# Kernel tuning notes

Hardware: AMD Instinct MI355X
Metric: run time of the kernel (lower is better)

## Reference

```python
import jax, jax.numpy as jnp
import numpy as np

C = 512
GROUPS = 8
EPS = 1e-5


def setup_inputs() -> dict:
    key = jax.random.key(0)
    ks = jax.random.split(key, 7)
    B, H, W = 16, 32, 32
    x = jax.random.normal(ks[0], (B, C, H, W), dtype=jnp.float32)
    gamma = jnp.ones((C,), jnp.float32)
    beta = jnp.zeros((C,), jnp.float32)
    # 1x1 convs stored as [out, in] matrices
    w_qkv = jax.random.normal(ks[1], (3 * C, C), dtype=jnp.float32) * (1.0 / np.sqrt(C))
    b_qkv = jax.random.normal(ks[2], (3 * C,), dtype=jnp.float32) * 0.02
    w_proj = jax.random.normal(ks[3], (C, C), dtype=jnp.float32) * (1.0 / np.sqrt(C))
    b_proj = jax.random.normal(ks[4], (C,), dtype=jnp.float32) * 0.02
    return {"x": x, "gamma": gamma, "beta": beta, "w_qkv": w_qkv,
            "b_qkv": b_qkv, "w_proj": w_proj, "b_proj": b_proj}


def _group_norm(x, gamma, beta):
    B, Cc, H, W = x.shape
    xg = x.reshape(B, GROUPS, Cc // GROUPS, H, W)
    mean = xg.mean(axis=(2, 3, 4), keepdims=True)
    var = xg.var(axis=(2, 3, 4), keepdims=True)
    xg = (xg - mean) * jax.lax.rsqrt(var + EPS)
    x = xg.reshape(B, Cc, H, W)
    return x * gamma[None, :, None, None] + beta[None, :, None, None]


def reference(x, gamma, beta, w_qkv, b_qkv, w_proj, b_proj):
    B, Cc, H, W = x.shape
    N = H * W
    h = _group_norm(x, gamma, beta)  # [B,C,H,W]
    hf = h.reshape(B, Cc, N)  # [B,C,N]
    # 1x1 conv == matmul over channel dim
    qkv = jnp.einsum('oc,bcn->bon', w_qkv, hf) + b_qkv[None, :, None]  # [B,3C,N]
    q, k, v = jnp.split(qkv, 3, axis=1)  # each [B,C,N]
    scale = 1.0 / jnp.sqrt(jnp.float32(Cc))
    # attn[b,i,j] = sum_c q[b,c,i] * k[b,c,j]
    attn = jnp.einsum('bci,bcj->bij', q, k) * scale  # [B,N,N]
    attn = jax.nn.softmax(attn, axis=-1)
    out = jnp.einsum('bij,bcj->bci', attn, v)  # [B,C,N]
    out = jnp.einsum('oc,bcn->bon', w_proj, out) + b_proj[None, :, None]
    return x + out.reshape(B, Cc, H, W)
```

## Files before the change

kernel.cpp:

```cpp
#include <hip/hip_runtime.h>
#include <hip/hip_bf16.h>

typedef unsigned short u16;
typedef unsigned int u32;
typedef __attribute__((ext_vector_type(8))) short short8;
typedef __attribute__((ext_vector_type(4))) float floatx4;

#define BATCH 16
#define CDIM 512
#define NSPAT 1024
#define NGROUP 8

__device__ __forceinline__ u16 f2bf(float f) {
    unsigned u = __float_as_uint(f);
    u += 0x7FFFu + ((u >> 16) & 1u);
    return (u16)(u >> 16);
}
__device__ __forceinline__ u32 f2bf2(float lo, float hi) {
    __hip_bfloat162 h = __float22bfloat162_rn(make_float2(lo, hi));
    return *(u32*)&h;
}

__device__ __forceinline__ void load_lds16(const void* g, void* l) {
    __builtin_amdgcn_global_load_lds(
        (const __attribute__((address_space(1))) unsigned int*)g,
        (__attribute__((address_space(3))) unsigned int*)l, 16, 0, 0);
}

__global__ __launch_bounds__(256) void prep_kernel(
    const float* __restrict__ w_qkv, const float* __restrict__ w_proj,
    const float* __restrict__ b_qkv, const float* __restrict__ x,
    u16* __restrict__ wmega, u16* __restrict__ wproj_bf, u16* __restrict__ wv_t,
    float* __restrict__ stats, float* __restrict__ lsums, float* __restrict__ bpv) {
    int b = blockIdx.x;
    int tid = threadIdx.x;
    if (b < 768) {
        const float* src = (b < 512) ? w_qkv : w_proj;
        u16* dst = (b < 512) ? wmega : wproj_bf;
        int i = (b < 512 ? b : b - 512) * 256 + tid;
        float4 v = ((const float4*)src)[i];
        u32* d = (u32*)dst;
        d[i * 2] = f2bf2(v.x, v.y);
        d[i * 2 + 1] = f2bf2(v.z, v.w);
        return;
    }
    if (b < 832) {
        __shared__ u16 t[64 * 66];
        int bt = b - 768;
        int tx = bt & 7, ty = bt >> 3;
        const float* src = w_qkv + (size_t)(1024 + ty * 64) * CDIM + tx * 64;
#pragma unroll
        for (int p = 0; p < 4; ++p) {
            int r = p * 16 + (tid >> 4);
            int c4 = (tid & 15) << 2;
            float4 v = *(const float4*)(src + (size_t)r * CDIM + c4);
            u16* d = &t[r * 66 + c4];
            d[0] = f2bf(v.x); d[1] = f2bf(v.y); d[2] = f2bf(v.z); d[3] = f2bf(v.w);
        }
        __syncthreads();
        u16* dst = wv_t + (size_t)(tx * 64) * CDIM + ty * 64;
#pragma unroll
        for (int p = 0; p < 4; ++p) {
            int c = p * 16 + (tid >> 4);
            int r4 = (tid & 15) << 2;
            ushort4 o;
            o.x = t[(r4 + 0) * 66 + c];
            o.y = t[(r4 + 1) * 66 + c];
            o.z = t[(r4 + 2) * 66 + c];
            o.w = t[(r4 + 3) * 66 + c];
            *(ushort4*)(dst + (size_t)c * CDIM + r4) = o;
        }
        return;
    }
    if (b < 960) {
        __shared__ float rs[4], rss[4];
        int bg = b - 832;
        const float4* xv = (const float4*)(x + (size_t)bg * 65536);
        float s = 0.f, ss = 0.f;
        for (int i = tid; i < 16384; i += 256) {
            float4 v = xv[i];
            s += v.x + v.y + v.z + v.w;
            ss += v.x * v.x + v.y * v.y + v.z * v.z + v.w * v.w;
        }
#pragma unroll
        for (int off = 32; off; off >>= 1) { s += __shfl_down(s, off); ss += __shfl_down(ss, off); }
        int wave = tid >> 6, lane = tid & 63;
        if (lane == 0) { rs[wave] = s; rss[wave] = ss; }
        __syncthreads();
        if (tid == 0) {
            float S1 = rs[0] + rs[1] + rs[2] + rs[3];
            float S2 = rss[0] + rss[1] + rss[2] + rss[3];
            float mean = S1 * (1.f / 65536.f);
            float var = S2 * (1.f / 65536.f) - mean * mean;
            stats[bg * 2] = mean;
            stats[bg * 2 + 1] = rsqrtf(var + 1e-5f);
        }
        return;
    }
    if (b < 976) {
        ((float4*)lsums)[(b - 960) * 256 + tid] = (float4){0.f, 0.f, 0.f, 0.f};
        return;
    }
    {
        int o0 = (b - 976) * 64;
        int wave = tid >> 6, lane = tid & 63;
        const float4* bvv = (const float4*)(b_qkv + 1024);
        float4 v0 = bvv[lane * 2], v1 = bvv[lane * 2 + 1];
        for (int it = 0; it < 16; ++it) {
            int o = o0 + wave * 16 + it;
            const float4* wr = (const float4*)(w_proj + (size_t)o * CDIM);
            float4 a0 = wr[lane * 2], a1 = wr[lane * 2 + 1];
            float s = a0.x * v0.x + a0.y * v0.y + a0.z * v0.z + a0.w * v0.w
                    + a1.x * v1.x + a1.y * v1.y + a1.z * v1.z + a1.w * v1.w;
#pragma unroll
            for (int off = 32; off; off >>= 1) s += __shfl_down(s, off);
            if (lane == 0) bpv[o] = s;
        }
    }
}

__device__ __forceinline__ void stage_tile(
    const u16* __restrict__ Ab, const u16* __restrict__ Bb, int lda, int ldb,
    int m0, int n0, int k0, u16* As, u16* Bs) {
    int tid = threadIdx.x;
#pragma unroll
    for (int it = 0; it < 4; ++it) {
        int c = it * 256 + tid;
        int r = c >> 3, p = c & 7;
        int kc = p ^ (r & 7);
        load_lds16(Ab + (size_t)(m0 + r) * lda + k0 + (kc << 3), &As[c << 3]);
        load_lds16(Bb + (size_t)(n0 + r) * ldb + k0 + (kc << 3), &Bs[c << 3]);
    }
}

__device__ __forceinline__ void compute_tile(
    const u16* As, const u16* Bs, int wm, int wn, int quad, int lrow,
    floatx4 (&acc)[4][4]) {
#pragma unroll
    for (int s = 0; s < 2; ++s) {
        short8 af[4], bf[4];
#pragma unroll
        for (int i = 0; i < 4; ++i) {
            int R = wm + i * 16 + lrow;
            int p = (s * 4 + quad) ^ (R & 7);
            af[i] = *(const short8*)&As[(R << 6) + (p << 3)];
        }
#pragma unroll
        for (int j = 0; j < 4; ++j) {
            int R = wn + j * 16 + lrow;
            int p = (s * 4 + quad) ^ (R & 7);
            bf[j] = *(const short8*)&Bs[(R << 6) + (p << 3)];
        }
#pragma unroll
        for (int i = 0; i < 4; ++i)
#pragma unroll
            for (int j = 0; j < 4; ++j)
                acc[i][j] = __builtin_amdgcn_mfma_f32_16x16x32_bf16(af[i], bf[j], acc[i][j], 0, 0, 0);
    }
}

__device__ __forceinline__ void gemm_core_sb(
    const u16* __restrict__ Ab, const u16* __restrict__ Bb, int K, int lda, int ldb,
    int m0, int n0, u16* As, u16* Bs, floatx4 (&acc)[4][4]) {
    int tid = threadIdx.x;
    int lane = tid & 63, wave = tid >> 6, quad = lane >> 4, lrow = lane & 15;
    int wm = (wave >> 1) << 6, wn = (wave & 1) << 6;
    for (int k0 = 0; k0 < K; k0 += 64) {
        stage_tile(Ab, Bb, lda, ldb, m0, n0, k0, As, Bs);
        __syncthreads();
        compute_tile(As, Bs, wm, wn, quad, lrow, acc);
        __syncthreads();
    }
}

#define ACC_INIT floatx4 acc[4][4]; \
    _Pragma("unroll") for (int i = 0; i < 4; ++i) \
    _Pragma("unroll") for (int j = 0; j < 4; ++j) acc[i][j] = (floatx4){0.f, 0.f, 0.f, 0.f};

#define EPILOG_IDX int lane = threadIdx.x & 63, wave = threadIdx.x >> 6; \
    int quad = lane >> 4, lrow = lane & 15; \
    int wm = (wave >> 1) << 6, wn = (wave & 1) << 6;

#define TSA 16384
#define TSB 8192

__device__ __forceinline__ void issueA(
    const u16* __restrict__ Ab, int lda, int m0, int t, int h, u16* smem) {
    int tid = threadIdx.x;
    u16* base = smem + (t & 1) * TSA + h * 8192;
#pragma unroll
    for (int l = 0; l < 2; ++l) {
        int c = l * 512 + tid;
        int ridx = c >> 3, p = c & 7;
        int kc = p ^ (ridx & 7);
        int r = ((ridx >> 6) << 7) + (h << 6) + (ridx & 63);
        load_lds16(Ab + (size_t)(m0 + r) * lda + (t << 6) + (kc << 3), base + (c << 3));
    }
}

__device__ __forceinline__ void issueB(
    const u16* __restrict__ Bb, int ldb, int n0, int t, int h, u16* smem) {
    int tid = threadIdx.x;
    u16* base = smem + 2 * TSA + (t & 1) * TSB + h * 4096;
    int ridx = tid >> 3, p = tid & 7;
    int kc = p ^ (ridx & 7);
    int r = ((ridx >> 4) << 5) + (h << 4) + (ridx & 15);
    load_lds16(Bb + (size_t)(n0 + r) * ldb + (t << 6) + (kc << 3), base + (tid << 3));
}

__device__ __forceinline__ void comp_phase(
    const u16* smem, int slot, int qm, int qn,
    int wrow, int wcol, int quad, int lrow, floatx4 (&acc)[8][2]) {
    const u16* Abase = smem + slot * TSA + qm * 8192;
    const u16* Bbase = smem + 2 * TSA + slot * TSB + qn * 4096;
    short8 af[8];
    short8 bf[2];
#pragma unroll
    for (int ks = 0; ks < 2; ++ks) {
#pragma unroll
        for (int i = 0; i < 4; ++i) {
            int ridx = wrow * 64 + i * 16 + lrow;
            int p = (ks * 4 + quad) ^ (ridx & 7);
            af[ks * 4 + i] = *(const short8*)&Abase[(ridx << 6) + (p << 3)];
        }
        int ridxb = wcol * 16 + lrow;
        int pb = (ks * 4 + quad) ^ (ridxb & 7);
        bf[ks] = *(const short8*)&Bbase[(ridxb << 6) + (pb << 3)];
    }
    asm volatile("s_waitcnt lgkmcnt(0)" ::: "memory");
    __builtin_amdgcn_sched_barrier(0);
    __builtin_amdgcn_s_setprio(1);
#pragma unroll
    for (int ks = 0; ks < 2; ++ks)
#pragma unroll
        for (int i = 0; i < 4; ++i)
            acc[qm * 4 + i][qn] = __builtin_amdgcn_mfma_f32_16x16x32_bf16(
                af[ks * 4 + i], bf[ks], acc[qm * 4 + i][qn], 0, 0, 0);
    __builtin_amdgcn_s_setprio(0);
}

#define PHASE_BAR  __builtin_amdgcn_s_barrier(); __builtin_amdgcn_sched_barrier(0);

__device__ __forceinline__ void gemm256(
    const u16* __restrict__ Ab, const u16* __restrict__ Bb, int K, int lda, int ldb,
    int m0, int n0, u16* smem, floatx4 (&acc)[8][2]) {
    int tid = threadIdx.x;
    int lane = tid & 63, wave = tid >> 6;
    int quad = lane >> 4, lrow = lane & 15;
    int wrow = wave >> 2, wcol = wave & 3;
    int nt = K >> 6;
    issueA(Ab, lda, m0, 0, 0, smem);
    issueA(Ab, lda, m0, 0, 1, smem);
    issueB(Bb, ldb, n0, 0, 0, smem);
    issueB(Bb, ldb, n0, 0, 1, smem);
    issueA(Ab, lda, m0, 1, 0, smem);
    issueB(Bb, ldb, n0, 1, 0, smem);
    for (int t = 0; t < nt; ++t) {
        int slot = t & 1;
        if (t + 1 < nt) { asm volatile("s_waitcnt vmcnt(3)" ::: "memory"); }
        else            { asm volatile("s_waitcnt vmcnt(0)" ::: "memory"); }
        PHASE_BAR;
        if (t + 1 < nt) issueA(Ab, lda, m0, t + 1, 1, smem);
        comp_phase(smem, slot, 0, 0, wrow, wcol, quad, lrow, acc);
        PHASE_BAR;
        if (t + 1 < nt) issueB(Bb, ldb, n0, t + 1, 1, smem);
        comp_phase(smem, slot, 0, 1, wrow, wcol, quad, lrow, acc);
        PHASE_BAR;
        if (t + 2 < nt) issueA(Ab, lda, m0, t + 2, 0, smem);
        comp_phase(smem, slot, 1, 0, wrow, wcol, quad, lrow, acc);
        PHASE_BAR;
        if (t + 2 < nt) issueB(Bb, ldb, n0, t + 2, 0, smem);
        comp_phase(smem, slot, 1, 1, wrow, wcol, quad, lrow, acc);
    }
    __builtin_amdgcn_sched_barrier(0);
}

#define ACC_INIT8 floatx4 acc[8][2]; \
    _Pragma("unroll") for (int i = 0; i < 8; ++i) \
    _Pragma("unroll") for (int j = 0; j < 2; ++j) acc[i][j] = (floatx4){0.f, 0.f, 0.f, 0.f};

#define EPILOG_IDX8 int lane = threadIdx.x & 63, wave = threadIdx.x >> 6; \
    int quad = lane >> 4, lrow = lane & 15; \
    int wrow = wave >> 2, wcol = wave & 3;

#define TSTR 66
__global__ __launch_bounds__(256) void gn_wpv_kernel(
    const float* __restrict__ x, const float* __restrict__ gamma, const float* __restrict__ beta,
    const float* __restrict__ stats, u16* __restrict__ hT,
    const u16* __restrict__ wproj_bf, const u16* __restrict__ wv_t, u16* __restrict__ wmega) {
    __shared__ u16 smem[2 * 128 * 64];
    int tid = threadIdx.x;
    if (blockIdx.z == 16) {
        if (blockIdx.x >= 4 || blockIdx.y >= 4) return;
        int m0 = blockIdx.y << 7, n0 = blockIdx.x << 7;
        ACC_INIT;
        gemm_core_sb(wproj_bf, wv_t, CDIM, CDIM, CDIM, m0, n0, smem, smem + 128 * 64, acc);
        EPILOG_IDX;
#pragma unroll
        for (int i = 0; i < 4; ++i)
#pragma unroll
            for (int j = 0; j < 4; ++j)
#pragma unroll
                for (int r = 0; r < 4; ++r) {
                    int R = m0 + wm + i * 16 + (quad << 2) + r;
                    int Cc = n0 + wn + j * 16 + lrow;
                    wmega[(size_t)(1024 + R) * CDIM + Cc] = f2bf(acc[i][j][r]);
                }
        return;
    }
    u16* t = smem;
    int b = blockIdx.z, c0 = blockIdx.y << 6, n0 = blockIdx.x << 6;
    const float* xb = x + ((size_t)b * CDIM + c0) * NSPAT + n0;
#pragma unroll
    for (int p = 0; p < 4; ++p) {
        int cl = p * 16 + (tid >> 4);
        int nl = (tid & 15) << 2;
        int c = c0 + cl;
        int bg = b * NGROUP + (c >> 6);
        float ga = gamma[c] * stats[bg * 2 + 1];
        float be = beta[c] - stats[bg * 2] * ga;
        float4 v = *(const float4*)(xb + (size_t)cl * NSPAT + nl);
        u16* dst = &t[cl * TSTR + nl];
        dst[0] = f2bf(v.x * ga + be);
        dst[1] = f2bf(v.y * ga + be);
        dst[2] = f2bf(v.z * ga + be);
        dst[3] = f2bf(v.w * ga + be);
    }
    __syncthreads();
    u16* hb = hT + ((size_t)b * NSPAT + n0) * CDIM + c0;
#pragma unroll
    for (int p = 0; p < 4; ++p) {
        int nl = p * 16 + (tid >> 4);
        int cl4 = (tid & 15) << 2;
        ushort4 o;
        o.x = t[(cl4 + 0) * TSTR + nl];
        o.y = t[(cl4 + 1) * TSTR + nl];
        o.z = t[(cl4 + 2) * TSTR + nl];
        o.w = t[(cl4 + 3) * TSTR + nl];
        *(ushort4*)(hb + (size_t)nl * CDIM + cl4) = o;
    }
}

__global__ __launch_bounds__(512, 2) void qkv_kernel(
    const u16* __restrict__ wmega, const u16* __restrict__ hT,
    const float* __restrict__ b_qkv, const float* __restrict__ bpv,
    u16* __restrict__ qkT, u16* __restrict__ WV) {
    extern __shared__ u16 smem[];
    int z = blockIdx.x;
    int n0 = blockIdx.y << 7;
    int m0 = blockIdx.z << 8;
    const u16* Bb = hT + (size_t)z * CDIM * NSPAT;
    ACC_INIT8;
    gemm256(wmega, Bb, CDIM, CDIM, CDIM, m0, n0, smem, acc);
    EPILOG_IDX8;
    if (blockIdx.z < 4) {
        u16* qk = qkT + (size_t)z * NSPAT * NSPAT;
#pragma unroll
        for (int mf = 0; mf < 8; ++mf)
#pragma unroll
            for (int nf = 0; nf < 2; ++nf) {
                int R0 = m0 + wrow * 128 + mf * 16 + (quad << 2);
                int Cc = n0 + wcol * 32 + nf * 16 + lrow;
                uint2 u;
                u.x = f2bf2(acc[mf][nf][0] + b_qkv[R0 + 0], acc[mf][nf][1] + b_qkv[R0 + 1]);
                u.y = f2bf2(acc[mf][nf][2] + b_qkv[R0 + 2], acc[mf][nf][3] + b_qkv[R0 + 3]);
                *(uint2*)&qk[(size_t)Cc * NSPAT + R0] = u;
            }
    } else {
        u16* Wp = WV + (size_t)z * CDIM * NSPAT;
#pragma unroll
        for (int mf = 0; mf < 8; ++mf)
#pragma unroll
            for (int nf = 0; nf < 2; ++nf)
#pragma unroll
                for (int r = 0; r < 4; ++r) {
                    int R = m0 - 1024 + wrow * 128 + mf * 16 + (quad << 2) + r;
                    int Cc = n0 + wcol * 32 + nf * 16 + lrow;
                    Wp[(size_t)R * NSPAT + Cc] = f2bf(acc[mf][nf][r] + bpv[R]);
                }
    }
}

__global__ __launch_bounds__(512, 2) void scores_kernel(
    const u16* __restrict__ qkT, u16* __restrict__ P, float* __restrict__ lsums, float scale) {
    extern __shared__ u16 smem[];
    int z = blockIdx.x;
    int n0 = blockIdx.y << 7;
    int m0 = blockIdx.z << 8;
    const u16* qb = qkT + (size_t)z * NSPAT * NSPAT;
    ACC_INIT8;
    gemm256(qb + CDIM, qb, CDIM, NSPAT, NSPAT, m0, n0, smem, acc);
    EPILOG_IDX8;
    u16* Pp = P + (size_t)z * NSPAT * NSPAT;
    float* ls = lsums + (size_t)z * NSPAT;
#pragma unroll
    for (int nf = 0; nf < 2; ++nf) {
        int Ci = n0 + wcol * 32 + nf * 16 + lrow;
        float part = 0.f;
#pragma unroll
        for (int mf = 0; mf < 8; ++mf) {
            int Rj0 = m0 + wrow * 128 + mf * 16 + (quad << 2);
            float e0 = __expf(acc[mf][nf][0] * scale);
            float e1 = __expf(acc[mf][nf][1] * scale);
            float e2 = __expf(acc[mf][nf][2] * scale);
            float e3 = __expf(acc[mf][nf][3] * scale);
            part += (e0 + e1) + (e2 + e3);
            uint2 u;
            u.x = f2bf2(e0, e1);
            u.y = f2bf2(e2, e3);
            *(uint2*)&Pp[(size_t)Ci * NSPAT + Rj0] = u;
        }
        part += __shfl_xor(part, 16);
        part += __shfl_xor(part, 32);
        if (lane < 16) atomicAdd(&ls[Ci], part);
    }
}

__global__ __launch_bounds__(512, 2) void final_kernel(
    const u16* __restrict__ WV, const u16* __restrict__ P, const float* __restrict__ lsums,
    const float* __restrict__ bias, const float* __restrict__ x, float* __restrict__ out) {
    extern __shared__ u16 smem[];
    int z = blockIdx.x;
    int n0 = blockIdx.y << 7;
    int m0 = blockIdx.z << 8;
    const u16* Pb = P + (size_t)z * NSPAT * NSPAT;
    const u16* WVb = WV + (size_t)z * CDIM * NSPAT;
    ACC_INIT8;
    gemm256(Pb, WVb, NSPAT, NSPAT, NSPAT, m0, n0, smem, acc);
    EPILOG_IDX8;
    float* Op = out + (size_t)z * CDIM * NSPAT;
    const float* xr = x + (size_t)z * CDIM * NSPAT;
    const float* li = lsums + (size_t)z * NSPAT;
#pragma unroll
    for (int mf = 0; mf < 8; ++mf) {
        int Ri0 = m0 + wrow * 128 + mf * 16 + (quad << 2);
        float4 lv = *(const float4*)&li[Ri0];
        float s0 = __builtin_amdgcn_rcpf(lv.x);
        float s1 = __builtin_amdgcn_rcpf(lv.y);
        float s2 = __builtin_amdgcn_rcpf(lv.z);
        float s3 = __builtin_amdgcn_rcpf(lv.w);
#pragma unroll
        for (int nf = 0; nf < 2; ++nf) {
            int Co = n0 + wcol * 32 + nf * 16 + lrow;
            float bv = bias[Co];
            size_t off = (size_t)Co * NSPAT + Ri0;
            float4 xv = *(const float4*)&xr[off];
            float4 o;
            o.x = acc[mf][nf][0] * s0 + bv + xv.x;
            o.y = acc[mf][nf][1] * s1 + bv + xv.y;
            o.z = acc[mf][nf][2] * s2 + bv + xv.z;
            o.w = acc[mf][nf][3] * s3 + bv + xv.w;
            *(float4*)&Op[off] = o;
        }
    }
}

extern "C" void kernel_launch(void* const* d_in, const int* in_sizes, int n_in,
                              void* d_out, int out_size, void* d_ws, size_t ws_size,
                              hipStream_t stream) {
    const float* x      = (const float*)d_in[0];
    const float* gamma  = (const float*)d_in[1];
    const float* beta   = (const float*)d_in[2];
    const float* w_qkv  = (const float*)d_in[3];
    const float* b_qkv  = (const float*)d_in[4];
    const float* w_proj = (const float*)d_in[5];
    const float* b_proj = (const float*)d_in[6];
    float* out = (float*)d_out;

    const size_t CN = (size_t)CDIM * NSPAT;
    const size_t NN = (size_t)NSPAT * NSPAT;
    const float SCALE = 0.044194173824159216f;
    const int LDS_BYTES = 2 * (TSA + TSB) * 2;

    char* ws = (char*)d_ws;
    float* stats   = (float*)ws;
    float* bpv     = (float*)(ws + 1024);
    u16* wmega     = (u16*)(ws + 4096);
    u16* wproj_bf  = wmega + (size_t)3 * CDIM * CDIM;
    u16* wv_t      = wproj_bf + (size_t)CDIM * CDIM;
    u16* hT        = wv_t + (size_t)CDIM * CDIM;
    u16* qkT       = hT + BATCH * CN;
    u16* WV        = qkT + BATCH * NN;
    u16* P         = WV + BATCH * CN;
    float* lsums   = (float*)(P + BATCH * NN);

    prep_kernel<<<984, 256, 0, stream>>>(
        w_qkv, w_proj, b_qkv, x, wmega, wproj_bf, wv_t, stats, lsums, bpv);

    gn_wpv_kernel<<<dim3(16, 8, 17), 256, 0, stream>>>(
        x, gamma, beta, stats, hT, wproj_bf, wv_t, wmega);

    qkv_kernel<<<dim3(BATCH, 8, 6), 512, LDS_BYTES, stream>>>(
        wmega, hT, b_qkv, bpv, qkT, WV);

    scores_kernel<<<dim3(BATCH, 8, 4), 512, LDS_BYTES, stream>>>(qkT, P, lsums, SCALE);

    final_kernel<<<dim3(BATCH, 4, 4), 512, LDS_BYTES, stream>>>(WV, P, lsums, b_proj, x, out);
}
```

Baseline: 149.9 us.

## Enlarge GEMM tiles to 256x256 for qkv/scores and 256x128 for final

Replaces the shared 256x128 pipelined GEMM with a 256x256 tile variant for the qkv and scores kernels and a 256x128 variant with full-K A staging for the final kernel. A-fragments are reused across two B sub-phases, and the wait counts and staging order are reworked for the new layout. Dynamic LDS grows to 128KB/96KB, set through hipFuncSetAttribute, and the epilogues load biases as float4. Larger tiles raise arithmetic intensity per LDS byte but halve the grid size and lower occupancy, which may hurt load balance across CUs.

```diff
diff --git a/kernel.cpp b/kernel.cpp
--- a/kernel.cpp
+++ b/kernel.cpp
@@ -26,6 +26,9 @@
         (const __attribute__((address_space(1))) unsigned int*)g,
         (__attribute__((address_space(3))) unsigned int*)l, 16, 0, 0);
 }
+
+#define SBAR0 __builtin_amdgcn_sched_barrier(0)
+#define BARRIER { SBAR0; __builtin_amdgcn_s_barrier(); SBAR0; }
 
 __global__ __launch_bounds__(256) void prep_kernel(
     const float* __restrict__ w_qkv, const float* __restrict__ w_proj,
@@ -181,107 +184,206 @@
     int quad = lane >> 4, lrow = lane & 15; \
     int wm = (wave >> 1) << 6, wn = (wave & 1) << 6;
 
-#define TSA 16384
-#define TSB 8192
-
-__device__ __forceinline__ void issueA(
+__device__ __forceinline__ void issueA2(
     const u16* __restrict__ Ab, int lda, int m0, int t, int h, u16* smem) {
     int tid = threadIdx.x;
-    u16* base = smem + (t & 1) * TSA + h * 8192;
+    u16* base = smem + (t & 1) * 16384 + h * 8192;
 #pragma unroll
     for (int l = 0; l < 2; ++l) {
         int c = l * 512 + tid;
-        int ridx = c >> 3, p = c & 7;
-        int kc = p ^ (ridx & 7);
-        int r = ((ridx >> 6) << 7) + (h << 6) + (ridx & 63);
+        int rho = c >> 3, p = c & 7;
+        int kc = p ^ (rho & 7);
+        int r = ((rho >> 6) << 7) | (h << 6) | (rho & 63);
         load_lds16(Ab + (size_t)(m0 + r) * lda + (t << 6) + (kc << 3), base + (c << 3));
     }
 }
-
-__device__ __forceinline__ void issueB(
+__device__ __forceinline__ void issueB2(
     const u16* __restrict__ Bb, int ldb, int n0, int t, int h, u16* smem) {
     int tid = threadIdx.x;
-    u16* base = smem + 2 * TSA + (t & 1) * TSB + h * 4096;
-    int ridx = tid >> 3, p = tid & 7;
-    int kc = p ^ (ridx & 7);
-    int r = ((ridx >> 4) << 5) + (h << 4) + (ridx & 15);
-    load_lds16(Bb + (size_t)(n0 + r) * ldb + (t << 6) + (kc << 3), base + (tid << 3));
-}
-
-__device__ __forceinline__ void comp_phase(
-    const u16* smem, int slot, int qm, int qn,
-    int wrow, int wcol, int quad, int lrow, floatx4 (&acc)[8][2]) {
-    const u16* Abase = smem + slot * TSA + qm * 8192;
-    const u16* Bbase = smem + 2 * TSA + slot * TSB + qn * 4096;
-    short8 af[8];
-    short8 bf[2];
+    u16* base = smem + 32768 + (t & 1) * 16384 + h * 8192;
+#pragma unroll
+    for (int l = 0; l < 2; ++l) {
+        int c = l * 512 + tid;
+        int rho = c >> 3, p = c & 7;
+        int kc = p ^ (rho & 7);
+        int r = ((rho >> 5) << 6) | (h << 5) | (rho & 31);
+        load_lds16(Bb + (size_t)(n0 + r) * ldb + (t << 6) + (kc << 3), base + (c << 3));
+    }
+}
+
+template <bool RD_AF, int QM, int QN>
+__device__ __forceinline__ void comp2(
+    const u16* smem, int slot, int wrow, int wcol, int quad, int lrow,
+    short8 (&af)[8], floatx4 (&acc)[8][4]) {
+    const u16* Ah = smem + slot * 16384 + QM * 8192;
+    const u16* Bh = smem + 32768 + slot * 16384 + QN * 8192;
+    short8 bf[4];
 #pragma unroll
     for (int ks = 0; ks < 2; ++ks) {
-#pragma unroll
-        for (int i = 0; i < 4; ++i) {
-            int ridx = wrow * 64 + i * 16 + lrow;
-            int p = (ks * 4 + quad) ^ (ridx & 7);
-            af[ks * 4 + i] = *(const short8*)&Abase[(ridx << 6) + (p << 3)];
-        }
-        int ridxb = wcol * 16 + lrow;
-        int pb = (ks * 4 + quad) ^ (ridxb & 7);
-        bf[ks] = *(const short8*)&Bbase[(ridxb << 6) + (pb << 3)];
+        if (RD_AF) {
+#pragma unroll
+            for (int i = 0; i < 4; ++i) {
+                int rho = wrow * 64 + i * 16 + lrow;
+                int p = (ks * 4 + quad) ^ (lrow & 7);
+                af[ks * 4 + i] = *(const short8*)&Ah[(rho << 6) + (p << 3)];
+            }
+        }
+#pragma unroll
+        for (int j = 0; j < 2; ++j) {
+            int rho = wcol * 32 + j * 16 + lrow;
+            int p = (ks * 4 + quad) ^ (lrow & 7);
+            bf[ks * 2 + j] = *(const short8*)&Bh[(rho << 6) + (p << 3)];
+        }
     }
     asm volatile("s_waitcnt lgkmcnt(0)" ::: "memory");
-    __builtin_amdgcn_sched_barrier(0);
+    SBAR0;
     __builtin_amdgcn_s_setprio(1);
 #pragma unroll
     for (int ks = 0; ks < 2; ++ks)
 #pragma unroll
         for (int i = 0; i < 4; ++i)
-            acc[qm * 4 + i][qn] = __builtin_amdgcn_mfma_f32_16x16x32_bf16(
-                af[ks * 4 + i], bf[ks], acc[qm * 4 + i][qn], 0, 0, 0);
+#pragma unroll
+            for (int j = 0; j < 2; ++j)
+                acc[QM * 4 + i][QN * 2 + j] = __builtin_amdgcn_mfma_f32_16x16x32_bf16(
+                    af[ks * 4 + i], bf[ks * 2 + j], acc[QM * 4 + i][QN * 2 + j], 0, 0, 0);
     __builtin_amdgcn_s_setprio(0);
 }
 
-#define PHASE_BAR  __builtin_amdgcn_s_barrier(); __builtin_amdgcn_sched_barrier(0);
-
-__device__ __forceinline__ void gemm256(
+__device__ __forceinline__ void gemm256x256(
     const u16* __restrict__ Ab, const u16* __restrict__ Bb, int K, int lda, int ldb,
-    int m0, int n0, u16* smem, floatx4 (&acc)[8][2]) {
+    int m0, int n0, u16* smem, floatx4 (&acc)[8][4]) {
     int tid = threadIdx.x;
     int lane = tid & 63, wave = tid >> 6;
     int quad = lane >> 4, lrow = lane & 15;
     int wrow = wave >> 2, wcol = wave & 3;
     int nt = K >> 6;
-    issueA(Ab, lda, m0, 0, 0, smem);
-    issueA(Ab, lda, m0, 0, 1, smem);
-    issueB(Bb, ldb, n0, 0, 0, smem);
-    issueB(Bb, ldb, n0, 0, 1, smem);
-    issueA(Ab, lda, m0, 1, 0, smem);
-    issueB(Bb, ldb, n0, 1, 0, smem);
+    short8 af[8];
+    issueA2(Ab, lda, m0, 0, 0, smem);
+    issueB2(Bb, ldb, n0, 0, 0, smem);
+    issueB2(Bb, ldb, n0, 0, 1, smem);
+    issueA2(Ab, lda, m0, 0, 1, smem);
     for (int t = 0; t < nt; ++t) {
         int slot = t & 1;
-        if (t + 1 < nt) { asm volatile("s_waitcnt vmcnt(3)" ::: "memory"); }
-        else            { asm volatile("s_waitcnt vmcnt(0)" ::: "memory"); }
-        PHASE_BAR;
-        if (t + 1 < nt) issueA(Ab, lda, m0, t + 1, 1, smem);
-        comp_phase(smem, slot, 0, 0, wrow, wcol, quad, lrow, acc);
-        PHASE_BAR;
-        if (t + 1 < nt) issueB(Bb, ldb, n0, t + 1, 1, smem);
-        comp_phase(smem, slot, 0, 1, wrow, wcol, quad, lrow, acc);
-        PHASE_BAR;
-        if (t + 2 < nt) issueA(Ab, lda, m0, t + 2, 0, smem);
-        comp_phase(smem, slot, 1, 0, wrow, wcol, quad, lrow, acc);
-        PHASE_BAR;
-        if (t + 2 < nt) issueB(Bb, ldb, n0, t + 2, 0, smem);
-        comp_phase(smem, slot, 1, 1, wrow, wcol, quad, lrow, acc);
-    }
-    __builtin_amdgcn_sched_barrier(0);
-}
-
-#define ACC_INIT8 floatx4 acc[8][2]; \
+        bool nxt = (t + 1 < nt);
+        asm volatile("s_waitcnt vmcnt(4)" ::: "memory");
+        BARRIER;
+        if (nxt) issueA2(Ab, lda, m0, t + 1, 0, smem);
+        comp2<true, 0, 0>(smem, slot, wrow, wcol, quad, lrow, af, acc);
+        BARRIER;
+        if (nxt) { asm volatile("s_waitcnt vmcnt(4)" ::: "memory"); }
+        else     { asm volatile("s_waitcnt vmcnt(2)" ::: "memory"); }
+        BARRIER;
+        if (nxt) issueB2(Bb, ldb, n0, t + 1, 0, smem);
+        comp2<false, 0, 1>(smem, slot, wrow, wcol, quad, lrow, af, acc);
+        BARRIER;
+        if (nxt) { asm volatile("s_waitcnt vmcnt(4)" ::: "memory"); }
+        else     { asm volatile("s_waitcnt vmcnt(0)" ::: "memory"); }
+        BARRIER;
+        if (nxt) issueB2(Bb, ldb, n0, t + 1, 1, smem);
+        comp2<true, 1, 0>(smem, slot, wrow, wcol, quad, lrow, af, acc);
+        BARRIER;
+        if (nxt) issueA2(Ab, lda, m0, t + 1, 1, smem);
+        comp2<false, 1, 1>(smem, slot, wrow, wcol, quad, lrow, af, acc);
+        BARRIER;
+    }
+}
+
+__device__ __forceinline__ void issueA4(
+    const u16* __restrict__ Ab, int lda, int m0, int t, u16* smem) {
+    int tid = threadIdx.x;
+    u16* base = smem + (t & 1) * 16384;
+#pragma unroll
+    for (int l = 0; l < 4; ++l) {
+        int c = l * 512 + tid;
+        int rho = c >> 3, p = c & 7;
+        int kc = p ^ (rho & 7);
+        load_lds16(Ab + (size_t)(m0 + rho) * lda + (t << 6) + (kc << 3), base + (c << 3));
+    }
+}
+__device__ __forceinline__ void issueB4(
+    const u16* __restrict__ Bb, int ldb, int n0, int t, int h, u16* smem) {
+    int tid = threadIdx.x;
+    u16* base = smem + 32768 + (t & 1) * 8192 + h * 4096;
+    int rho = tid >> 3, p = tid & 7;
+    int kc = p ^ (rho & 7);
+    int r = ((rho >> 5) << 6) | (h << 5) | (rho & 31);
+    load_lds16(Bb + (size_t)(n0 + r) * ldb + (t << 6) + (kc << 3), base + (tid << 3));
+}
+
+template <bool RD_AF, int QN>
+__device__ __forceinline__ void comp4(
+    const u16* smem, int slot, int wrow, int wcol, int quad, int lrow,
+    short8 (&af)[8], floatx4 (&acc)[4][4]) {
+    const u16* Ah = smem + slot * 16384;
+    const u16* Bh = smem + 32768 + slot * 8192 + QN * 4096;
+    short8 bf[4];
+#pragma unroll
+    for (int ks = 0; ks < 2; ++ks) {
+        if (RD_AF) {
+#pragma unroll
+            for (int i = 0; i < 4; ++i) {
+                int rho = wrow * 64 + i * 16 + lrow;
+                int p = (ks * 4 + quad) ^ (lrow & 7);
+                af[ks * 4 + i] = *(const short8*)&Ah[(rho << 6) + (p << 3)];
+            }
+        }
+#pragma unroll
+        for (int j = 0; j < 2; ++j) {
+            int rho = wcol * 32 + j * 16 + lrow;
+            int p = (ks * 4 + quad) ^ (lrow & 7);
+            bf[ks * 2 + j] = *(const short8*)&Bh[(rho << 6) + (p << 3)];
+        }
+    }
+    asm volatile("s_waitcnt lgkmcnt(0)" ::: "memory");
+    SBAR0;
+    __builtin_amdgcn_s_setprio(1);
+#pragma unroll
+    for (int ks = 0; ks < 2; ++ks)
+#pragma unroll
+        for (int i = 0; i < 4; ++i)
+#pragma unroll
+            for (int j = 0; j < 2; ++j)
+                acc[i][QN * 2 + j] = __builtin_amdgcn_mfma_f32_16x16x32_bf16(
+                    af[ks * 4 + i], bf[ks * 2 + j], acc[i][QN * 2 + j], 0, 0, 0);
+    __builtin_amdgcn_s_setprio(0);
+}
+
+__device__ __forceinline__ void gemm256x128(
+    const u16* __restrict__ Ab, const u16* __restrict__ Bb, int K, int lda, int ldb,
+    int m0, int n0, u16* smem, floatx4 (&acc)[4][4]) {
+    int tid = threadIdx.x;
+    int lane = tid & 63, wave = tid >> 6;
+    int quad = lane >> 4, lrow = lane & 15;
+    int wrow = wave >> 1, wcol = wave & 1;
+    int nt = K >> 6;
+    short8 af[8];
+    issueB4(Bb, ldb, n0, 0, 0, smem);
+    issueA4(Ab, lda, m0, 0, smem);
+    issueB4(Bb, ldb, n0, 0, 1, smem);
+    for (int t = 0; t < nt; ++t) {
+        int slot = t & 1;
+        bool nxt = (t + 1 < nt);
+        asm volatile("s_waitcnt vmcnt(1)" ::: "memory");
+        BARRIER;
+        if (nxt) { issueB4(Bb, ldb, n0, t + 1, 0, smem); issueA4(Ab, lda, m0, t + 1, smem); }
+        comp4<true, 0>(smem, slot, wrow, wcol, quad, lrow, af, acc);
+        BARRIER;
+        if (nxt) { asm volatile("s_waitcnt vmcnt(5)" ::: "memory"); }
+        else     { asm volatile("s_waitcnt vmcnt(0)" ::: "memory"); }
+        BARRIER;
+        if (nxt) issueB4(Bb, ldb, n0, t + 1, 1, smem);
+        comp4<false, 1>(smem, slot, wrow, wcol, quad, lrow, af, acc);
+        BARRIER;
+    }
+}
+
+#define ACC_INIT84 floatx4 acc[8][4]; \
     _Pragma("unroll") for (int i = 0; i < 8; ++i) \
-    _Pragma("unroll") for (int j = 0; j < 2; ++j) acc[i][j] = (floatx4){0.f, 0.f, 0.f, 0.f};
-
-#define EPILOG_IDX8 int lane = threadIdx.x & 63, wave = threadIdx.x >> 6; \
-    int quad = lane >> 4, lrow = lane & 15; \
-    int wrow = wave >> 2, wcol = wave & 3;
+    _Pragma("unroll") for (int j = 0; j < 4; ++j) acc[i][j] = (floatx4){0.f, 0.f, 0.f, 0.f};
+
+#define ACC_INIT44 floatx4 acc[4][4]; \
+    _Pragma("unroll") for (int i = 0; i < 4; ++i) \
+    _Pragma("unroll") for (int j = 0; j < 4; ++j) acc[i][j] = (floatx4){0.f, 0.f, 0.f, 0.f};
 
 #define TSTR 66
 __global__ __launch_bounds__(256) void gn_wpv_kernel(
@@ -347,37 +449,44 @@
     u16* __restrict__ qkT, u16* __restrict__ WV) {
     extern __shared__ u16 smem[];
     int z = blockIdx.x;
-    int n0 = blockIdx.y << 7;
+    int n0 = blockIdx.y << 8;
     int m0 = blockIdx.z << 8;
     const u16* Bb = hT + (size_t)z * CDIM * NSPAT;
-    ACC_INIT8;
-    gemm256(wmega, Bb, CDIM, CDIM, CDIM, m0, n0, smem, acc);
-    EPILOG_IDX8;
+    ACC_INIT84;
+    gemm256x256(wmega, Bb, CDIM, CDIM, CDIM, m0, n0, smem, acc);
+    int lane = threadIdx.x & 63, wave = threadIdx.x >> 6;
+    int quad = lane >> 4, lrow = lane & 15;
+    int wrow = wave >> 2, wcol = wave & 3;
     if (blockIdx.z < 4) {
         u16* qk = qkT + (size_t)z * NSPAT * NSPAT;
 #pragma unroll
-        for (int mf = 0; mf < 8; ++mf)
-#pragma unroll
-            for (int nf = 0; nf < 2; ++nf) {
-                int R0 = m0 + wrow * 128 + mf * 16 + (quad << 2);
-                int Cc = n0 + wcol * 32 + nf * 16 + lrow;
+        for (int mf = 0; mf < 8; ++mf) {
+            int R0 = m0 + wrow * 128 + mf * 16 + (quad << 2);
+            float4 bv = *(const float4*)&b_qkv[R0];
+#pragma unroll
+            for (int nf = 0; nf < 4; ++nf) {
+                int Cc = n0 + wcol * 64 + nf * 16 + lrow;
                 uint2 u;
-                u.x = f2bf2(acc[mf][nf][0] + b_qkv[R0 + 0], acc[mf][nf][1] + b_qkv[R0 + 1]);
-                u.y = f2bf2(acc[mf][nf][2] + b_qkv[R0 + 2], acc[mf][nf][3] + b_qkv[R0 + 3]);
+                u.x = f2bf2(acc[mf][nf][0] + bv.x, acc[mf][nf][1] + bv.y);
+                u.y = f2bf2(acc[mf][nf][2] + bv.z, acc[mf][nf][3] + bv.w);
                 *(uint2*)&qk[(size_t)Cc * NSPAT + R0] = u;
             }
+        }
     } else {
         u16* Wp = WV + (size_t)z * CDIM * NSPAT;
 #pragma unroll
-        for (int mf = 0; mf < 8; ++mf)
-#pragma unroll
-            for (int nf = 0; nf < 2; ++nf)
-#pragma unroll
-                for (int r = 0; r < 4; ++r) {
-                    int R = m0 - 1024 + wrow * 128 + mf * 16 + (quad << 2) + r;
-                    int Cc = n0 + wcol * 32 + nf * 16 + lrow;
-                    Wp[(size_t)R * NSPAT + Cc] = f2bf(acc[mf][nf][r] + bpv[R]);
-                }
+        for (int mf = 0; mf < 8; ++mf) {
+            int R = m0 - 1024 + wrow * 128 + mf * 16 + (quad << 2);
+            float4 pv = *(const float4*)&bpv[R];
+#pragma unroll
+            for (int nf = 0; nf < 4; ++nf) {
+                int Cc = n0 + wcol * 64 + nf * 16 + lrow;
+                Wp[(size_t)(R + 0) * NSPAT + Cc] = f2bf(acc[mf][nf][0] + pv.x);
+                Wp[(size_t)(R + 1) * NSPAT + Cc] = f2bf(acc[mf][nf][1] + pv.y);
+                Wp[(size_t)(R + 2) * NSPAT + Cc] = f2bf(acc[mf][nf][2] + pv.z);
+                Wp[(size_t)(R + 3) * NSPAT + Cc] = f2bf(acc[mf][nf][3] + pv.w);
+            }
+        }
     }
 }
 
@@ -385,17 +494,19 @@
     const u16* __restrict__ qkT, u16* __restrict__ P, float* __restrict__ lsums, float scale) {
     extern __shared__ u16 smem[];
     int z = blockIdx.x;
-    int n0 = blockIdx.y << 7;
+    int n0 = blockIdx.y << 8;
     int m0 = blockIdx.z << 8;
     const u16* qb = qkT + (size_t)z * NSPAT * NSPAT;
-    ACC_INIT8;
-    gemm256(qb + CDIM, qb, CDIM, NSPAT, NSPAT, m0, n0, smem, acc);
-    EPILOG_IDX8;
+    ACC_INIT84;
+    gemm256x256(qb + CDIM, qb, CDIM, NSPAT, NSPAT, m0, n0, smem, acc);
+    int lane = threadIdx.x & 63, wave = threadIdx.x >> 6;
+    int quad = lane >> 4, lrow = lane & 15;
+    int wrow = wave >> 2, wcol = wave & 3;
     u16* Pp = P + (size_t)z * NSPAT * NSPAT;
     float* ls = lsums + (size_t)z * NSPAT;
 #pragma unroll
-    for (int nf = 0; nf < 2; ++nf) {
-        int Ci = n0 + wcol * 32 + nf * 16 + lrow;
+    for (int nf = 0; nf < 4; ++nf) {
+        int Ci = n0 + wcol * 64 + nf * 16 + lrow;
         float part = 0.f;
 #pragma unroll
         for (int mf = 0; mf < 8; ++mf) {
@@ -425,23 +536,25 @@
     int m0 = blockIdx.z << 8;
     const u16* Pb = P + (size_t)z * NSPAT * NSPAT;
     const u16* WVb = WV + (size_t)z * CDIM * NSPAT;
-    ACC_INIT8;
-    gemm256(Pb, WVb, NSPAT, NSPAT, NSPAT, m0, n0, smem, acc);
-    EPILOG_IDX8;
+    ACC_INIT44;
+    gemm256x128(Pb, WVb, NSPAT, NSPAT, NSPAT, m0, n0, smem, acc);
+    int lane = threadIdx.x & 63, wave = threadIdx.x >> 6;
+    int quad = lane >> 4, lrow = lane & 15;
+    int wrow = wave >> 1, wcol = wave & 1;
     float* Op = out + (size_t)z * CDIM * NSPAT;
     const float* xr = x + (size_t)z * CDIM * NSPAT;
     const float* li = lsums + (size_t)z * NSPAT;
 #pragma unroll
-    for (int mf = 0; mf < 8; ++mf) {
-        int Ri0 = m0 + wrow * 128 + mf * 16 + (quad << 2);
+    for (int mf = 0; mf < 4; ++mf) {
+        int Ri0 = m0 + wrow * 64 + mf * 16 + (quad << 2);
         float4 lv = *(const float4*)&li[Ri0];
         float s0 = __builtin_amdgcn_rcpf(lv.x);
         float s1 = __builtin_amdgcn_rcpf(lv.y);
         float s2 = __builtin_amdgcn_rcpf(lv.z);
         float s3 = __builtin_amdgcn_rcpf(lv.w);
 #pragma unroll
-        for (int nf = 0; nf < 2; ++nf) {
-            int Co = n0 + wcol * 32 + nf * 16 + lrow;
+        for (int nf = 0; nf < 4; ++nf) {
+            int Co = n0 + wcol * 64 + nf * 16 + lrow;
             float bv = bias[Co];
             size_t off = (size_t)Co * NSPAT + Ri0;
             float4 xv = *(const float4*)&xr[off];
@@ -470,7 +583,19 @@
     const size_t CN = (size_t)CDIM * NSPAT;
     const size_t NN = (size_t)NSPAT * NSPAT;
     const float SCALE = 0.044194173824159216f;
-    const int LDS_BYTES = 2 * (TSA + TSB) * 2;
+    const int LDS_BIG = 131072;
+    const int LDS_MED = 98304;
+
+    static bool lds_attr_done = false;
+    if (!lds_attr_done) {
+        hipFuncSetAttribute((const void*)qkv_kernel,
+                            hipFuncAttributeMaxDynamicSharedMemorySize, LDS_BIG);
+        hipFuncSetAttribute((const void*)scores_kernel,
+                            hipFuncAttributeMaxDynamicSharedMemorySize, LDS_BIG);
+        hipFuncSetAttribute((const void*)final_kernel,
+                            hipFuncAttributeMaxDynamicSharedMemorySize, LDS_MED);
+        lds_attr_done = true;
+    }
 
     char* ws = (char*)d_ws;
     float* stats   = (float*)ws;
@@ -490,10 +615,10 @@
     gn_wpv_kernel<<<dim3(16, 8, 17), 256, 0, stream>>>(
         x, gamma, beta, stats, hT, wproj_bf, wv_t, wmega);
 
-    qkv_kernel<<<dim3(BATCH, 8, 6), 512, LDS_BYTES, stream>>>(
+    qkv_kernel<<<dim3(BATCH, 4, 6), 512, LDS_BIG, stream>>>(
         wmega, hT, b_qkv, bpv, qkT, WV);
 
-    scores_kernel<<<dim3(BATCH, 8, 4), 512, LDS_BYTES, stream>>>(qkT, P, lsums, SCALE);
-
-    final_kernel<<<dim3(BATCH, 4, 4), 512, LDS_BYTES, stream>>>(WV, P, lsums, b_proj, x, out);
-}
+    scores_kernel<<<dim3(BATCH, 4, 4), 512, LDS_BIG, stream>>>(qkT, P, lsums, SCALE);
+
+    final_kernel<<<dim3(BATCH, 4, 4), 512, LDS_MED, stream>>>(WV, P, lsums, b_proj, x, out);
+}
```

Result: faster. 138.7 us (-7.5%).
